# Performance work log

Hardware: AMD Instinct MI355X
Metric: run time of the kernel (lower is better)

## Reference

```python
import jax, jax.numpy as jnp
import numpy as np

NEG_SLOPE_ATTN = 0.2   # DGL GATConv attention leaky_relu slope
NEG_SLOPE_ACT = 0.01   # nn.LeakyReLU() default activation slope


def _gat_layer(h, src, dst, W, al, ar, b, activate):
    """One DGL-style GATConv. h: [N, F_in]; W: [F_in, H*D]; al/ar: [H, D]; b: [H*D].
    Returns [N, H, D]."""
    N = h.shape[0]
    H, D = al.shape
    feat = (h @ W).reshape(N, H, D)                      # [N, H, D]
    el = jnp.sum(feat * al, axis=-1)                     # [N, H] source term
    er = jnp.sum(feat * ar, axis=-1)                     # [N, H] dest term
    e = jax.nn.leaky_relu(el[src] + er[dst], NEG_SLOPE_ATTN)  # [E, H]
    # segment softmax over destination nodes
    m = jax.ops.segment_max(e, dst, num_segments=N)      # [N, H]
    ex = jnp.exp(e - m[dst])                             # [E, H]
    s = jax.ops.segment_sum(ex, dst, num_segments=N)     # [N, H]
    alpha = ex / s[dst]                                  # [E, H]
    msg = feat[src] * alpha[..., None]                   # [E, H, D]
    out = jax.ops.segment_sum(msg, dst, num_segments=N)  # [N, H, D]
    out = out + b.reshape(H, D)
    if activate:
        out = jax.nn.leaky_relu(out, NEG_SLOPE_ACT)
    return out


def setup_inputs() -> dict:
    key = jax.random.key(0)
    ks = jax.random.split(key, 16)
    N, E, IN = 50000, 800000, 128
    H, D = 2, 128
    HD = H * D
    lin = lambda k, fi, fo: (jax.random.normal(k, (fi, fo), jnp.float32) / np.sqrt(fi).astype(np.float32))
    att = lambda k, h, d: jax.random.normal(k, (h, d), jnp.float32) * 0.1
    return {
        "features": jax.random.normal(ks[0], (N, IN), jnp.float32),
        "src": jax.random.randint(ks[1], (E,), 0, N),
        "dst": jax.random.randint(ks[2], (E,), 0, N),
        "W0": lin(ks[3], IN, HD), "al0": att(ks[4], H, D), "ar0": att(ks[5], H, D), "b0": jnp.zeros((HD,), jnp.float32),
        "W1": lin(ks[6], HD, HD), "al1": att(ks[7], H, D), "ar1": att(ks[8], H, D), "b1": jnp.zeros((HD,), jnp.float32),
        "W2": lin(ks[9], HD, 1), "al2": att(ks[10], 1, 1), "ar2": att(ks[11], 1, 1), "b2": jnp.zeros((1,), jnp.float32),
    }


def reference(features, src, dst, W0, al0, ar0, b0, W1, al1, ar1, b1, W2, al2, ar2, b2):
    N = features.shape[0]
    # hidden GAT layers with head flattening (dropout is identity in eval mode)
    h = _gat_layer(features, src, dst, W0, al0, ar0, b0, True).reshape(N, -1)
    h = _gat_layer(h, src, dst, W1, al1, ar1, b1, True).reshape(N, -1)
    # final single-head, out_feats=1, no activation
    out = _gat_layer(h, src, dst, W2, al2, ar2, b2, False)  # [N, 1, 1]
    return out.squeeze(), h
```

## Files before the change

### kernel.cpp

```cpp
#include <hip/hip_runtime.h>
#include <hip/hip_fp16.h>
#include <math.h>


#define NEG_ATTN 0.2f
#define NEG_ACT  0.01f

typedef short bf16x8 __attribute__((ext_vector_type(8)));
typedef float f32x4  __attribute__((ext_vector_type(4)));
typedef unsigned short ushort_t;

__device__ inline void bf16split(float x, unsigned short& h, unsigned short& l) {
    unsigned b = __float_as_uint(x);
    h = (unsigned short)(b >> 16);
    float hf = __uint_as_float(b & 0xFFFF0000u);
    l = (unsigned short)(__float_as_uint(x - hf) >> 16);
}


__global__ void count_edges(const int* __restrict__ dst, int* __restrict__ counts, int E) {
    int e = blockIdx.x * blockDim.x + threadIdx.x;
    if (e < E) atomicAdd(&counts[dst[e]], 1);
}

__global__ __launch_bounds__(256) void scan_phase1(
    const int* __restrict__ in, int* __restrict__ out1 ,
    int* __restrict__ bsum, int n)
{
    __shared__ int wsum[4];
    int i = blockIdx.x * 256 + threadIdx.x;
    int lane = threadIdx.x & 63, wv = threadIdx.x >> 6;
    int v = (i < n) ? in[i] : 0;
    int x = v;
    #pragma unroll
    for (int off = 1; off < 64; off <<= 1) {
        int y = __shfl_up(x, off);
        if (lane >= off) x += y;
    }
    if (lane == 63) wsum[wv] = x;
    __syncthreads();
    int add = 0;
    for (int w = 0; w < wv; ++w) add += wsum[w];
    x += add;
    if (i < n) out1[i] = x;
    if (threadIdx.x == 255) bsum[blockIdx.x] = x;
}

__global__ __launch_bounds__(256) void scan_phase2(int* __restrict__ bsum, int nb) {
    __shared__ int wsum[4];
    int t = threadIdx.x;
    int lane = t & 63, wv = t >> 6;
    int x = (t < nb) ? bsum[t] : 0;
    #pragma unroll
    for (int off = 1; off < 64; off <<= 1) {
        int y = __shfl_up(x, off);
        if (lane >= off) x += y;
    }
    if (lane == 63) wsum[wv] = x;
    __syncthreads();
    int add = 0;
    for (int w = 0; w < wv; ++w) add += wsum[w];
    x += add;
    if (t < nb) bsum[t] = x;
}

__global__ __launch_bounds__(256) void scan_phase3(
    int* __restrict__ out1, const int* __restrict__ bsum, int n)
{
    int i = blockIdx.x * 256 + threadIdx.x;
    int add = (blockIdx.x > 0) ? bsum[blockIdx.x - 1] : 0;
    if (i < n) out1[i] += add;
    if (i == 0) out1[-1] = 0;
}

__global__ void scatter_edges(const int* __restrict__ src, const int* __restrict__ dst,
                              const int* __restrict__ offsets, int* __restrict__ cursor,
                              int* __restrict__ csr_src, int E) {
    int e = blockIdx.x * blockDim.x + threadIdx.x;
    if (e < E) {
        int d = dst[e];
        int pos = offsets[d] + atomicAdd(&cursor[d], 1);
        csr_src[pos] = src[e];
    }
}


__global__ void transpose_w_bf16(const float* __restrict__ W,
                                 ushort_t* __restrict__ Wt_hi,
                                 ushort_t* __restrict__ Wt_lo, int K, int Nw) {
    int idx = blockIdx.x * blockDim.x + threadIdx.x;
    if (idx >= K * Nw) return;
    int k = idx / Nw, n = idx - k * Nw;
    unsigned short h, l;
    bf16split(W[idx], h, l);
    Wt_hi[(size_t)n * K + k] = h;
    Wt_lo[(size_t)n * K + k] = l;
}


__global__ void split_f32(const float* __restrict__ x,
                          ushort_t* __restrict__ hi, ushort_t* __restrict__ lo, int n4) {
    int i = blockIdx.x * blockDim.x + threadIdx.x;
    if (i >= n4) return;
    float4 v = reinterpret_cast<const float4*>(x)[i];
    ushort4 h, l;
    bf16split(v.x, h.x, l.x);
    bf16split(v.y, h.y, l.y);
    bf16split(v.z, h.z, l.z);
    bf16split(v.w, h.w, l.w);
    reinterpret_cast<ushort4*>(hi)[i] = h;
    reinterpret_cast<ushort4*>(lo)[i] = l;
}


__global__ __launch_bounds__(256) void gemm_bf16split(
    const ushort_t* __restrict__ Ah, const ushort_t* __restrict__ Al,
    const ushort_t* __restrict__ Bh, const ushort_t* __restrict__ Bl,
    const float* __restrict__ alf, const float* __restrict__ arf,
    __half* __restrict__ feat16, float* __restrict__ el, float* __restrict__ er,
    int M, int K)
{
    const int LDT = 72;
    __shared__ ushort_t As_hi[64][LDT], As_lo[64][LDT];
    __shared__ ushort_t Bs_hi[64][LDT], Bs_lo[64][LDT];

    int tid = threadIdx.x, wv = tid >> 6, lane = tid & 63;
    int bm = blockIdx.x * 64, bn = blockIdx.y * 64;
    int wr = wv >> 1, wc = wv & 1;

    f32x4 acc[2][2] = {};

    int srow = tid >> 2;
    int sc0  = (tid & 3) * 16;

    size_t abase = (size_t)min(bm + srow, M - 1) * K;
    size_t bbase = (size_t)(bn + srow) * K;

    int frow = lane & 15;
    int fkg  = (lane >> 4) * 8;

    for (int k0 = 0; k0 < K; k0 += 64) {
        #pragma unroll
        for (int j = 0; j < 2; ++j) {
            int c = sc0 + j * 8;
            *reinterpret_cast<uint4*>(&As_hi[srow][c]) =
                *reinterpret_cast<const uint4*>(&Ah[abase + k0 + c]);
            *reinterpret_cast<uint4*>(&As_lo[srow][c]) =
                *reinterpret_cast<const uint4*>(&Al[abase + k0 + c]);
            *reinterpret_cast<uint4*>(&Bs_hi[srow][c]) =
                *reinterpret_cast<const uint4*>(&Bh[bbase + k0 + c]);
            *reinterpret_cast<uint4*>(&Bs_lo[srow][c]) =
                *reinterpret_cast<const uint4*>(&Bl[bbase + k0 + c]);
        }
        __syncthreads();

        #pragma unroll
        for (int ks = 0; ks < 2; ++ks) {
            int kb = ks * 32 + fkg;
            bf16x8 ah[2], al_[2], bh[2], bl[2];
            #pragma unroll
            for (int i = 0; i < 2; ++i) {
                int r = wr * 32 + i * 16 + frow;
                ah[i]  = *reinterpret_cast<const bf16x8*>(&As_hi[r][kb]);
                al_[i] = *reinterpret_cast<const bf16x8*>(&As_lo[r][kb]);
            }
            #pragma unroll
            for (int j = 0; j < 2; ++j) {
                int r = wc * 32 + j * 16 + frow;
                bh[j] = *reinterpret_cast<const bf16x8*>(&Bs_hi[r][kb]);
                bl[j] = *reinterpret_cast<const bf16x8*>(&Bs_lo[r][kb]);
            }
            #pragma unroll
            for (int i = 0; i < 2; ++i)
                #pragma unroll
                for (int j = 0; j < 2; ++j) {
                    acc[i][j] = __builtin_amdgcn_mfma_f32_16x16x32_bf16(ah[i],  bh[j], acc[i][j], 0, 0, 0);
                    acc[i][j] = __builtin_amdgcn_mfma_f32_16x16x32_bf16(ah[i],  bl[j], acc[i][j], 0, 0, 0);
                    acc[i][j] = __builtin_amdgcn_mfma_f32_16x16x32_bf16(al_[i], bh[j], acc[i][j], 0, 0, 0);
                }
        }
        __syncthreads();
    }

    int colbase = bn + wc * 32;
    int c0 = colbase + (lane & 15);
    int c1 = c0 + 16;
    float alw0 = alf[c0], alw1 = alf[c1];
    float arw0 = arf[c0], arw1 = arf[c1];
    int hH = colbase >> 7;
    int g4 = (lane >> 4) * 4;
    int sub = lane & 15;

    #pragma unroll
    for (int i = 0; i < 2; ++i) {
        int row0 = bm + wr * 32 + i * 16 + g4;
        #pragma unroll
        for (int r = 0; r < 4; ++r) {
            int row = row0 + r;
            if (row < M) {
                feat16[(size_t)row * 256 + c0] = __float2half(acc[i][0][r]);
                feat16[(size_t)row * 256 + c1] = __float2half(acc[i][1][r]);
            }
        }
        float pel[4], per_[4];
        #pragma unroll
        for (int r = 0; r < 4; ++r) {
            pel[r]  = acc[i][0][r] * alw0 + acc[i][1][r] * alw1;
            per_[r] = acc[i][0][r] * arw0 + acc[i][1][r] * arw1;
        }
        #pragma unroll
        for (int off = 1; off < 16; off <<= 1) {
            #pragma unroll
            for (int r = 0; r < 4; ++r) {
                pel[r]  += __shfl_xor(pel[r], off);
                per_[r] += __shfl_xor(per_[r], off);
            }
        }
        if (sub < 4) {
            int row = row0 + sub;
            float v = (sub == 0) ? pel[0] : (sub == 1) ? pel[1] : (sub == 2) ? pel[2] : pel[3];
            if (row < M) atomicAdd(&el[(size_t)row * 2 + hH], v);
        } else if (sub < 8) {
            int r = sub - 4;
            int row = row0 + r;
            float v = (r == 0) ? per_[0] : (r == 1) ? per_[1] : (r == 2) ? per_[2] : per_[3];
            if (row < M) atomicAdd(&er[(size_t)row * 2 + hH], v);
        }
    }
}


__global__ __launch_bounds__(256) void gat_fused_agg(
    const __half* __restrict__ feat16, const float* __restrict__ el, const float* __restrict__ er,
    const int* __restrict__ offsets, const int* __restrict__ csr_src,
    const float* __restrict__ bias, float* __restrict__ out, int N, int activate,
    const float* __restrict__ W2, float* __restrict__ feat2,
    ushort_t* __restrict__ outHi, ushort_t* __restrict__ outLo)
{
    int wv = threadIdx.x >> 6, lane = threadIdx.x & 63;
    int n = blockIdx.x * 4 + wv;
    if (n >= N) return;
    int hsel = lane >> 5;
    int d4 = (lane & 31) * 4 + hsel * 128;
    const char* fbase = (const char*)feat16 + (size_t)d4 * 2;
    int p0 = offsets[n], p1 = offsets[n + 1];

    float2 ern = *reinterpret_cast<const float2*>(er + 2 * (size_t)n);
    const float NEG_INF = -__builtin_inff();
    float m0 = NEG_INF, m1 = NEG_INF, s0 = 0.f, s1 = 0.f;
    float4 acc = make_float4(0.f, 0.f, 0.f, 0.f);

    for (int base = p0; base < p1; base += 32) {
        int cnt = min(32, p1 - base);
        int cl = lane & 31;
        bool active = cl < cnt;
        int src_v = csr_src[base + min(cl, cnt - 1)];
        float ex = NEG_INF, ey = NEG_INF;
        if (active) {
            float2 e2 = *reinterpret_cast<const float2*>(el + 2 * (size_t)src_v);
            ex = e2.x + ern.x; ey = e2.y + ern.y;
            ex = (ex >= 0.f) ? ex : NEG_ATTN * ex;
            ey = (ey >= 0.f) ? ey : NEG_ATTN * ey;
        }
        float mc0 = ex, mc1 = ey;
        #pragma unroll
        for (int off = 16; off; off >>= 1) {
            mc0 = fmaxf(mc0, __shfl_xor(mc0, off));
            mc1 = fmaxf(mc1, __shfl_xor(mc1, off));
        }
        float nm0 = fmaxf(m0, mc0), nm1 = fmaxf(m1, mc1);
        float sc0 = __expf(m0 - nm0), sc1 = __expf(m1 - nm1);
        float wx = active ? __expf(ex - nm0) : 0.f;
        float wy = active ? __expf(ey - nm1) : 0.f;
        float sw0 = wx, sw1 = wy;
        #pragma unroll
        for (int off = 16; off; off >>= 1) {
            sw0 += __shfl_xor(sw0, off);
            sw1 += __shfl_xor(sw1, off);
        }
        s0 = s0 * sc0 + sw0;
        s1 = s1 * sc1 + sw1;
        float scH = hsel ? sc1 : sc0;
        acc.x *= scH; acc.y *= scH; acc.z *= scH; acc.w *= scH;
        m0 = nm0; m1 = nm1;

        int c = 0;
        for (; c + 4 <= cnt; c += 4) {
            int   i0 = __shfl(src_v, c);
            int   i1 = __shfl(src_v, c + 1);
            int   i2 = __shfl(src_v, c + 2);
            int   i3 = __shfl(src_v, c + 3);
            float ax0 = __shfl(wx, c),     ay0 = __shfl(wy, c);
            float ax1 = __shfl(wx, c + 1), ay1 = __shfl(wy, c + 1);
            float ax2 = __shfl(wx, c + 2), ay2 = __shfl(wy, c + 2);
            float ax3 = __shfl(wx, c + 3), ay3 = __shfl(wy, c + 3);
            float a0 = hsel ? ay0 : ax0;
            float a1 = hsel ? ay1 : ax1;
            float a2 = hsel ? ay2 : ax2;
            float a3 = hsel ? ay3 : ax3;
            uint2 r0 = *reinterpret_cast<const uint2*>(fbase + (size_t)i0 * 512);
            uint2 r1 = *reinterpret_cast<const uint2*>(fbase + (size_t)i1 * 512);
            uint2 r2 = *reinterpret_cast<const uint2*>(fbase + (size_t)i2 * 512);
            uint2 r3 = *reinterpret_cast<const uint2*>(fbase + (size_t)i3 * 512);
            {
                float2 fa = __half22float2(*reinterpret_cast<const __half2*>(&r0.x));
                float2 fb = __half22float2(*reinterpret_cast<const __half2*>(&r0.y));
                acc.x = fmaf(a0, fa.x, acc.x); acc.y = fmaf(a0, fa.y, acc.y);
                acc.z = fmaf(a0, fb.x, acc.z); acc.w = fmaf(a0, fb.y, acc.w);
            }
            {
                float2 fa = __half22float2(*reinterpret_cast<const __half2*>(&r1.x));
                float2 fb = __half22float2(*reinterpret_cast<const __half2*>(&r1.y));
                acc.x = fmaf(a1, fa.x, acc.x); acc.y = fmaf(a1, fa.y, acc.y);
                acc.z = fmaf(a1, fb.x, acc.z); acc.w = fmaf(a1, fb.y, acc.w);
            }
            {
                float2 fa = __half22float2(*reinterpret_cast<const __half2*>(&r2.x));
                float2 fb = __half22float2(*reinterpret_cast<const __half2*>(&r2.y));
                acc.x = fmaf(a2, fa.x, acc.x); acc.y = fmaf(a2, fa.y, acc.y);
                acc.z = fmaf(a2, fb.x, acc.z); acc.w = fmaf(a2, fb.y, acc.w);
            }
            {
                float2 fa = __half22float2(*reinterpret_cast<const __half2*>(&r3.x));
                float2 fb = __half22float2(*reinterpret_cast<const __half2*>(&r3.y));
                acc.x = fmaf(a3, fa.x, acc.x); acc.y = fmaf(a3, fa.y, acc.y);
                acc.z = fmaf(a3, fb.x, acc.z); acc.w = fmaf(a3, fb.y, acc.w);
            }
        }
        for (; c < cnt; ++c) {
            int   i0 = __shfl(src_v, c);
            float ax0 = __shfl(wx, c), ay0 = __shfl(wy, c);
            float a0 = hsel ? ay0 : ax0;
            uint2 r0 = *reinterpret_cast<const uint2*>(fbase + (size_t)i0 * 512);
            float2 fa = __half22float2(*reinterpret_cast<const __half2*>(&r0.x));
            float2 fb = __half22float2(*reinterpret_cast<const __half2*>(&r0.y));
            acc.x = fmaf(a0, fa.x, acc.x); acc.y = fmaf(a0, fa.y, acc.y);
            acc.z = fmaf(a0, fb.x, acc.z); acc.w = fmaf(a0, fb.y, acc.w);
        }
    }

    float inv0 = (s0 > 0.f) ? 1.f / s0 : 0.f;
    float inv1 = (s1 > 0.f) ? 1.f / s1 : 0.f;
    float inv = hsel ? inv1 : inv0;
    float4 b4 = *reinterpret_cast<const float4*>(bias + d4);
    acc.x = fmaf(acc.x, inv, b4.x);
    acc.y = fmaf(acc.y, inv, b4.y);
    acc.z = fmaf(acc.z, inv, b4.z);
    acc.w = fmaf(acc.w, inv, b4.w);
    if (activate) {
        acc.x = (acc.x >= 0.f) ? acc.x : NEG_ACT * acc.x;
        acc.y = (acc.y >= 0.f) ? acc.y : NEG_ACT * acc.y;
        acc.z = (acc.z >= 0.f) ? acc.z : NEG_ACT * acc.z;
        acc.w = (acc.w >= 0.f) ? acc.w : NEG_ACT * acc.w;
    }
    *reinterpret_cast<float4*>(out + (size_t)n * 256 + d4) = acc;

    if (outHi != nullptr) {
        ushort4 h, l;
        bf16split(acc.x, h.x, l.x);
        bf16split(acc.y, h.y, l.y);
        bf16split(acc.z, h.z, l.z);
        bf16split(acc.w, h.w, l.w);
        *reinterpret_cast<ushort4*>(outHi + (size_t)n * 256 + d4) = h;
        *reinterpret_cast<ushort4*>(outLo + (size_t)n * 256 + d4) = l;
    }

    if (W2 != nullptr) {
        float4 w4 = *reinterpret_cast<const float4*>(W2 + d4);
        float d = acc.x * w4.x + acc.y * w4.y + acc.z * w4.z + acc.w * w4.w;
        #pragma unroll
        for (int off = 32; off; off >>= 1) d += __shfl_xor(d, off);
        if (lane == 0) feat2[n] = d;
    }
}


__global__ __launch_bounds__(256) void gat_aggregate2_wave(
    const float* __restrict__ feat2, const float* __restrict__ al2, const float* __restrict__ ar2,
    const float* __restrict__ b2, const int* __restrict__ offsets, const int* __restrict__ csr_src,
    float* __restrict__ out, int N)
{
    int wv = threadIdx.x >> 6, lane = threadIdx.x & 63;
    int n = blockIdx.x * 4 + wv;
    if (n >= N) return;
    float alv = al2[0], arv = ar2[0];
    float ern = feat2[n] * arv;
    int p0 = offsets[n], p1 = offsets[n + 1];
    const float NEG_INF = -__builtin_inff();
    float m = NEG_INF, s = 0.f, acc = 0.f;

    for (int base = p0; base < p1; base += 64) {
        bool active = (base + lane) < p1;
        int sn = active ? csr_src[base + lane] : 0;
        float f = active ? feat2[sn] : 0.f;
        float e = NEG_INF;
        if (active) {
            e = fmaf(f, alv, ern);
            e = (e >= 0.f) ? e : NEG_ATTN * e;
        }
        float mc = e;
        #pragma unroll
        for (int off = 32; off; off >>= 1) mc = fmaxf(mc, __shfl_xor(mc, off));
        float nm = fmaxf(m, mc);
        float sc = __expf(m - nm);
        float w = active ? __expf(e - nm) : 0.f;
        s   = s * sc + w;
        acc = acc * sc + w * f;
        m = nm;
    }
    #pragma unroll
    for (int off = 32; off; off >>= 1) {
        s   += __shfl_xor(s, off);
        acc += __shfl_xor(acc, off);
    }
    if (lane == 0) out[n] = ((s > 0.f) ? acc / s : 0.f) + b2[0];
}


extern "C" void kernel_launch(void* const* d_in, const int* in_sizes, int n_in,
                              void* d_out, int out_size, void* d_ws, size_t ws_size,
                              hipStream_t stream)
{
    const float* features = (const float*)d_in[0];
    const int*   src      = (const int*)d_in[1];
    const int*   dst      = (const int*)d_in[2];
    const float* W0  = (const float*)d_in[3];
    const float* al0 = (const float*)d_in[4];
    const float* ar0 = (const float*)d_in[5];
    const float* b0  = (const float*)d_in[6];
    const float* W1  = (const float*)d_in[7];
    const float* al1 = (const float*)d_in[8];
    const float* ar1 = (const float*)d_in[9];
    const float* b1  = (const float*)d_in[10];
    const float* W2  = (const float*)d_in[11];
    const float* al2 = (const float*)d_in[12];
    const float* ar2 = (const float*)d_in[13];
    const float* b2  = (const float*)d_in[14];

    const int IN = 128, HD = 256;
    const int N = in_sizes[0] / IN;
    const int E = in_sizes[1];
    const int NB = (N + 255) / 256;

    float* out_final = (float*)d_out;
    float* h2        = (float*)d_out + N;

    char* ws = (char*)d_ws;
    size_t off = 0;
    auto alloc = [&](size_t bytes) { void* p = ws + off; off += (bytes + 255) & ~255ULL; return p; };
    __half*   featH  = (__half*)alloc((size_t)N * HD * 2);
    ushort_t* Fh     = (ushort_t*)alloc((size_t)N * IN * 2);
    ushort_t* Fl     = (ushort_t*)alloc((size_t)N * IN * 2);
    ushort_t* H1h    = (ushort_t*)alloc((size_t)N * HD * 2);
    ushort_t* H1l    = (ushort_t*)alloc((size_t)N * HD * 2);
    float*    el     = (float*)alloc((size_t)N * 2 * 4);
    float*    er     = (float*)alloc((size_t)N * 2 * 4);
    float*    feat2  = (float*)alloc((size_t)N * 4);
    int*      counts = (int*)alloc((size_t)N * 4);
    int*      cursor = (int*)alloc((size_t)N * 4);
    int*      offs   = (int*)alloc((size_t)(N + 1) * 4);
    int*      bsum   = (int*)alloc((size_t)NB * 4);
    int*      csr_src = (int*)alloc((size_t)E * 4);
    ushort_t* Wt0h = (ushort_t*)alloc((size_t)IN * HD * 2);
    ushort_t* Wt0l = (ushort_t*)alloc((size_t)IN * HD * 2);
    ushort_t* Wt1h = (ushort_t*)alloc((size_t)HD * HD * 2);
    ushort_t* Wt1l = (ushort_t*)alloc((size_t)HD * HD * 2);

    hipMemsetAsync(counts, 0, (size_t)N * 4, stream);
    hipMemsetAsync(cursor, 0, (size_t)N * 4, stream);

    transpose_w_bf16<<<(IN * HD + 255) / 256, 256, 0, stream>>>(W0, Wt0h, Wt0l, IN, HD);
    transpose_w_bf16<<<(HD * HD + 255) / 256, 256, 0, stream>>>(W1, Wt1h, Wt1l, HD, HD);
    split_f32<<<((N * IN / 4) + 255) / 256, 256, 0, stream>>>(features, Fh, Fl, N * IN / 4);

    count_edges<<<(E + 255) / 256, 256, 0, stream>>>(dst, counts, E);
    scan_phase1<<<NB, 256, 0, stream>>>(counts, offs + 1, bsum, N);
    scan_phase2<<<1, 256, 0, stream>>>(bsum, NB);
    scan_phase3<<<NB, 256, 0, stream>>>(offs + 1, bsum, N);
    scatter_edges<<<(E + 255) / 256, 256, 0, stream>>>(src, dst, offs, cursor, csr_src, E);

    dim3 gemm_grid((N + 63) / 64, HD / 64);

    hipMemsetAsync(el, 0, (size_t)N * 2 * 4, stream);
    hipMemsetAsync(er, 0, (size_t)N * 2 * 4, stream);
    gemm_bf16split<<<gemm_grid, 256, 0, stream>>>(Fh, Fl, Wt0h, Wt0l, al0, ar0,
                                                  featH, el, er, N, IN);
    gat_fused_agg<<<(N + 3) / 4, 256, 0, stream>>>(featH, el, er, offs, csr_src, b0,
                                                   h2, N, 1, nullptr, nullptr, H1h, H1l);

    hipMemsetAsync(el, 0, (size_t)N * 2 * 4, stream);
    hipMemsetAsync(er, 0, (size_t)N * 2 * 4, stream);
    gemm_bf16split<<<gemm_grid, 256, 0, stream>>>(H1h, H1l, Wt1h, Wt1l, al1, ar1,
                                                  featH, el, er, N, HD);
    gat_fused_agg<<<(N + 3) / 4, 256, 0, stream>>>(featH, el, er, offs, csr_src, b1,
                                                   h2, N, 1, W2, feat2, nullptr, nullptr);

    gat_aggregate2_wave<<<(N + 3) / 4, 256, 0, stream>>>(feat2, al2, ar2, b2, offs,
                                                         csr_src, out_final, N);
}
```

Measured before the change: 434.7 us.

## Compute full 256-wide GEMM row tile per block and drop el/er atomics

The GEMM now uses 512-thread blocks that each compute a 64x256 output tile, so every A tile is read once instead of four times. Per-head attention dot products are reduced in shared memory and written directly, which removes the el/er memsets and atomics. The first layer's fp32 output write is skipped because only the split bf16 copy is consumed. In exchange, the K step shrinks to 32, more shared memory is used for B, and the tile is covered by fewer, larger blocks.

New measurement: 405.9 us. 1.07x faster.

```diff
diff --git a/kernel.cpp b/kernel.cpp
--- a/kernel.cpp
+++ b/kernel.cpp
@@ -97,7 +97,6 @@
     Wt_lo[(size_t)n * K + k] = l;
 }
 
-
 __global__ void split_f32(const float* __restrict__ x,
                           ushort_t* __restrict__ hi, ushort_t* __restrict__ lo, int n4) {
     int i = blockIdx.x * blockDim.x + threadIdx.x;
@@ -113,83 +112,84 @@
 }
 
 
-__global__ __launch_bounds__(256) void gemm_bf16split(
+__global__ __launch_bounds__(512) void gemm_bn256(
     const ushort_t* __restrict__ Ah, const ushort_t* __restrict__ Al,
     const ushort_t* __restrict__ Bh, const ushort_t* __restrict__ Bl,
     const float* __restrict__ alf, const float* __restrict__ arf,
     __half* __restrict__ feat16, float* __restrict__ el, float* __restrict__ er,
     int M, int K)
 {
-    const int LDT = 72;
+    const int LDT = 40;
     __shared__ ushort_t As_hi[64][LDT], As_lo[64][LDT];
-    __shared__ ushort_t Bs_hi[64][LDT], Bs_lo[64][LDT];
+    __shared__ ushort_t Bs_hi[256][LDT], Bs_lo[256][LDT];
+    __shared__ float part_el[64][4], part_er[64][4];
 
     int tid = threadIdx.x, wv = tid >> 6, lane = tid & 63;
-    int bm = blockIdx.x * 64, bn = blockIdx.y * 64;
-    int wr = wv >> 1, wc = wv & 1;
-
-    f32x4 acc[2][2] = {};
-
-    int srow = tid >> 2;
-    int sc0  = (tid & 3) * 16;
-
-    size_t abase = (size_t)min(bm + srow, M - 1) * K;
-    size_t bbase = (size_t)(bn + srow) * K;
+    int bm = blockIdx.x * 64;
+    int wr = wv >> 2, wc = wv & 3;
+
+    f32x4 acc[2][4] = {};
+
+    int t2   = tid & 255;
+    int arow = t2 >> 2;
+    int akg  = (t2 & 3) * 8;
+    size_t abase = (size_t)min(bm + arow, M - 1) * K + akg;
+    int half = tid >> 8;
 
     int frow = lane & 15;
     int fkg  = (lane >> 4) * 8;
 
-    for (int k0 = 0; k0 < K; k0 += 64) {
+    for (int k0 = 0; k0 < K; k0 += 32) {
+        if (half == 0)
+            *reinterpret_cast<uint4*>(&As_hi[arow][akg]) =
+                *reinterpret_cast<const uint4*>(&Ah[abase + k0]);
+        else
+            *reinterpret_cast<uint4*>(&As_lo[arow][akg]) =
+                *reinterpret_cast<const uint4*>(&Al[abase + k0]);
         #pragma unroll
         for (int j = 0; j < 2; ++j) {
-            int c = sc0 + j * 8;
-            *reinterpret_cast<uint4*>(&As_hi[srow][c]) =
-                *reinterpret_cast<const uint4*>(&Ah[abase + k0 + c]);
-            *reinterpret_cast<uint4*>(&As_lo[srow][c]) =
-                *reinterpret_cast<const uint4*>(&Al[abase + k0 + c]);
-            *reinterpret_cast<uint4*>(&Bs_hi[srow][c]) =
-                *reinterpret_cast<const uint4*>(&Bh[bbase + k0 + c]);
-            *reinterpret_cast<uint4*>(&Bs_lo[srow][c]) =
-                *reinterpret_cast<const uint4*>(&Bl[bbase + k0 + c]);
+            int L = tid + 512 * j;
+            int brow = L >> 2, bkg = (L & 3) * 8;
+            size_t g = (size_t)brow * K + k0 + bkg;
+            *reinterpret_cast<uint4*>(&Bs_hi[brow][bkg]) =
+                *reinterpret_cast<const uint4*>(&Bh[g]);
+            *reinterpret_cast<uint4*>(&Bs_lo[brow][bkg]) =
+                *reinterpret_cast<const uint4*>(&Bl[g]);
         }
         __syncthreads();
 
-        #pragma unroll
-        for (int ks = 0; ks < 2; ++ks) {
-            int kb = ks * 32 + fkg;
-            bf16x8 ah[2], al_[2], bh[2], bl[2];
+        bf16x8 ah[2], al_[2], bh[4], bl[4];
+        #pragma unroll
+        for (int i = 0; i < 2; ++i) {
+            int r = wr * 32 + i * 16 + frow;
+            ah[i]  = *reinterpret_cast<const bf16x8*>(&As_hi[r][fkg]);
+            al_[i] = *reinterpret_cast<const bf16x8*>(&As_lo[r][fkg]);
+        }
+        #pragma unroll
+        for (int j = 0; j < 4; ++j) {
+            int c = wc * 64 + j * 16 + frow;
+            bh[j] = *reinterpret_cast<const bf16x8*>(&Bs_hi[c][fkg]);
+            bl[j] = *reinterpret_cast<const bf16x8*>(&Bs_lo[c][fkg]);
+        }
+        #pragma unroll
+        for (int i = 0; i < 2; ++i)
             #pragma unroll
-            for (int i = 0; i < 2; ++i) {
-                int r = wr * 32 + i * 16 + frow;
-                ah[i]  = *reinterpret_cast<const bf16x8*>(&As_hi[r][kb]);
-                al_[i] = *reinterpret_cast<const bf16x8*>(&As_lo[r][kb]);
-            }
-            #pragma unroll
-            for (int j = 0; j < 2; ++j) {
-                int r = wc * 32 + j * 16 + frow;
-                bh[j] = *reinterpret_cast<const bf16x8*>(&Bs_hi[r][kb]);
-                bl[j] = *reinterpret_cast<const bf16x8*>(&Bs_lo[r][kb]);
-            }
-            #pragma unroll
-            for (int i = 0; i < 2; ++i)
-                #pragma unroll
-                for (int j = 0; j < 2; ++j) {
-                    acc[i][j] = __builtin_amdgcn_mfma_f32_16x16x32_bf16(ah[i],  bh[j], acc[i][j], 0, 0, 0);
-                    acc[i][j] = __builtin_amdgcn_mfma_f32_16x16x32_bf16(ah[i],  bl[j], acc[i][j], 0, 0, 0);
-                    acc[i][j] = __builtin_amdgcn_mfma_f32_16x16x32_bf16(al_[i], bh[j], acc[i][j], 0, 0, 0);
-                }
-        }
+            for (int j = 0; j < 4; ++j) {
+                acc[i][j] = __builtin_amdgcn_mfma_f32_16x16x32_bf16(ah[i],  bh[j], acc[i][j], 0, 0, 0);
+                acc[i][j] = __builtin_amdgcn_mfma_f32_16x16x32_bf16(ah[i],  bl[j], acc[i][j], 0, 0, 0);
+                acc[i][j] = __builtin_amdgcn_mfma_f32_16x16x32_bf16(al_[i], bh[j], acc[i][j], 0, 0, 0);
+            }
         __syncthreads();
     }
 
-    int colbase = bn + wc * 32;
-    int c0 = colbase + (lane & 15);
-    int c1 = c0 + 16;
-    float alw0 = alf[c0], alw1 = alf[c1];
-    float arw0 = arf[c0], arw1 = arf[c1];
-    int hH = colbase >> 7;
     int g4 = (lane >> 4) * 4;
-    int sub = lane & 15;
+    float alw[4], arw[4];
+    #pragma unroll
+    for (int j = 0; j < 4; ++j) {
+        int c = wc * 64 + j * 16 + frow;
+        alw[j] = alf[c];
+        arw[j] = arf[c];
+    }
 
     #pragma unroll
     for (int i = 0; i < 2; ++i) {
@@ -198,15 +198,22 @@
         for (int r = 0; r < 4; ++r) {
             int row = row0 + r;
             if (row < M) {
-                feat16[(size_t)row * 256 + c0] = __float2half(acc[i][0][r]);
-                feat16[(size_t)row * 256 + c1] = __float2half(acc[i][1][r]);
+                #pragma unroll
+                for (int j = 0; j < 4; ++j)
+                    feat16[(size_t)row * 256 + wc * 64 + j * 16 + frow] =
+                        __float2half(acc[i][j][r]);
             }
         }
         float pel[4], per_[4];
         #pragma unroll
         for (int r = 0; r < 4; ++r) {
-            pel[r]  = acc[i][0][r] * alw0 + acc[i][1][r] * alw1;
-            per_[r] = acc[i][0][r] * arw0 + acc[i][1][r] * arw1;
+            float pe = 0.f, pr = 0.f;
+            #pragma unroll
+            for (int j = 0; j < 4; ++j) {
+                pe = fmaf(acc[i][j][r], alw[j], pe);
+                pr = fmaf(acc[i][j][r], arw[j], pr);
+            }
+            pel[r] = pe; per_[r] = pr;
         }
         #pragma unroll
         for (int off = 1; off < 16; off <<= 1) {
@@ -216,15 +223,28 @@
                 per_[r] += __shfl_xor(per_[r], off);
             }
         }
-        if (sub < 4) {
-            int row = row0 + sub;
-            float v = (sub == 0) ? pel[0] : (sub == 1) ? pel[1] : (sub == 2) ? pel[2] : pel[3];
-            if (row < M) atomicAdd(&el[(size_t)row * 2 + hH], v);
-        } else if (sub < 8) {
-            int r = sub - 4;
-            int row = row0 + r;
-            float v = (r == 0) ? per_[0] : (r == 1) ? per_[1] : (r == 2) ? per_[2] : per_[3];
-            if (row < M) atomicAdd(&er[(size_t)row * 2 + hH], v);
+        if (frow == 0) {
+            int lrow = wr * 32 + i * 16 + g4;
+            #pragma unroll
+            for (int r = 0; r < 4; ++r) {
+                part_el[lrow + r][wc] = pel[r];
+                part_er[lrow + r][wc] = per_[r];
+            }
+        }
+    }
+    __syncthreads();
+
+    if (tid < 256) {
+        int row = tid >> 2, which = tid & 3;
+        int grow = bm + row;
+        if (grow < M) {
+            float v;
+            if (which == 0)      v = part_el[row][0] + part_el[row][1];
+            else if (which == 1) v = part_el[row][2] + part_el[row][3];
+            else if (which == 2) v = part_er[row][0] + part_er[row][1];
+            else                 v = part_er[row][2] + part_er[row][3];
+            if (which < 2) el[(size_t)grow * 2 + which] = v;
+            else           er[(size_t)grow * 2 + (which - 2)] = v;
         }
     }
 }
@@ -353,7 +373,8 @@
         acc.z = (acc.z >= 0.f) ? acc.z : NEG_ACT * acc.z;
         acc.w = (acc.w >= 0.f) ? acc.w : NEG_ACT * acc.w;
     }
-    *reinterpret_cast<float4*>(out + (size_t)n * 256 + d4) = acc;
+    if (out != nullptr)
+        *reinterpret_cast<float4*>(out + (size_t)n * 256 + d4) = acc;
 
     if (outHi != nullptr) {
         ushort4 h, l;
@@ -479,19 +500,15 @@
     scan_phase3<<<NB, 256, 0, stream>>>(offs + 1, bsum, N);
     scatter_edges<<<(E + 255) / 256, 256, 0, stream>>>(src, dst, offs, cursor, csr_src, E);
 
-    dim3 gemm_grid((N + 63) / 64, HD / 64);
-
-    hipMemsetAsync(el, 0, (size_t)N * 2 * 4, stream);
-    hipMemsetAsync(er, 0, (size_t)N * 2 * 4, stream);
-    gemm_bf16split<<<gemm_grid, 256, 0, stream>>>(Fh, Fl, Wt0h, Wt0l, al0, ar0,
-                                                  featH, el, er, N, IN);
+    int gblocks = (N + 63) / 64;
+
+    gemm_bn256<<<gblocks, 512, 0, stream>>>(Fh, Fl, Wt0h, Wt0l, al0, ar0,
+                                            featH, el, er, N, IN);
     gat_fused_agg<<<(N + 3) / 4, 256, 0, stream>>>(featH, el, er, offs, csr_src, b0,
-                                                   h2, N, 1, nullptr, nullptr, H1h, H1l);
-
-    hipMemsetAsync(el, 0, (size_t)N * 2 * 4, stream);
-    hipMemsetAsync(er, 0, (size_t)N * 2 * 4, stream);
-    gemm_bf16split<<<gemm_grid, 256, 0, stream>>>(H1h, H1l, Wt1h, Wt1l, al1, ar1,
-                                                  featH, el, er, N, HD);
+                                                   nullptr, N, 1, nullptr, nullptr, H1h, H1l);
+
+    gemm_bn256<<<gblocks, 512, 0, stream>>>(H1h, H1l, Wt1h, Wt1l, al1, ar1,
+                                            featH, el, er, N, HD);
     gat_fused_agg<<<(N + 3) / 4, 256, 0, stream>>>(featH, el, er, offs, csr_src, b1,
                                                    h2, N, 1, W2, feat2, nullptr, nullptr);
 
```
